# Performance work log

Measured on AMD Instinct MI355X. Metric: run time of the kernel, lower is better.

Reference implementation:

```python
import jax, jax.numpy as jnp
import numpy as np

EMBED = 1024
HEADS = 16
HEAD_DIM = EMBED // HEADS


def setup_inputs() -> dict:
    key = jax.random.key(0)
    ks = jax.random.split(key, 9)
    s = 0.02
    return {
        "hidden_states": jax.random.normal(ks[0], (1, 4, 1500, EMBED), dtype=jnp.float32),
        "q_w": jax.random.normal(ks[1], (EMBED, EMBED), dtype=jnp.float32) * s,
        "q_b": jax.random.normal(ks[2], (EMBED,), dtype=jnp.float32) * s,
        "k_w": jax.random.normal(ks[3], (EMBED, EMBED), dtype=jnp.float32) * s,
        "v_w": jax.random.normal(ks[4], (EMBED, EMBED), dtype=jnp.float32) * s,
        "v_b": jax.random.normal(ks[5], (EMBED,), dtype=jnp.float32) * s,
        "out_w": jax.random.normal(ks[6], (EMBED, EMBED), dtype=jnp.float32) * s,
        "out_b": jax.random.normal(ks[7], (EMBED,), dtype=jnp.float32) * s,
    }


def reference(hidden_states, q_w, q_b, k_w, v_w, v_b, out_w, out_b):
    # hidden_states: [1, B, S, E]
    _, bsz, tgt_len, _ = hidden_states.shape
    x = hidden_states[0]  # [B, S, E]
    scaling = HEAD_DIM ** -0.5

    def split_heads(t):  # [B, S, E] -> [B, H, S, Dh]
        return t.reshape(bsz, tgt_len, HEADS, HEAD_DIM).transpose(0, 2, 1, 3)

    # Linear layers use torch convention: y = x @ W.T + b  (k_proj has no bias)
    q = split_heads((x @ q_w.T + q_b) * scaling)
    k = split_heads(x @ k_w.T)
    v = split_heads(x @ v_w.T + v_b)

    # attention scores [B, H, S, S]
    attn_weights = jnp.einsum("bhqd,bhkd->bhqk", q, k)
    attn_probs = jax.nn.softmax(attn_weights, axis=-1)
    attn_out = jnp.einsum("bhqk,bhkd->bhqd", attn_probs, v)  # [B, H, S, Dh]

    attn_out = attn_out.transpose(0, 2, 1, 3).reshape(1, bsz, tgt_len, EMBED)
    return attn_out @ out_w.T + out_b
```

## Files before the change

### kernel.cpp

```cpp
#include <hip/hip_runtime.h>
#include <cstddef>
#include <cstdint>

#define EMB 1024
#define SEQ 1500
#define NB 4
#define NH 16
#define DH 64
#define MTOT (NB*SEQ)
#define VTS 1536

typedef __bf16 bf16;
typedef __bf16 bf16x4 __attribute__((ext_vector_type(4)));
typedef __bf16 bf16x8 __attribute__((ext_vector_type(8)));
typedef short  s16x4  __attribute__((ext_vector_type(4)));
typedef float  f32x4  __attribute__((ext_vector_type(4)));

#define LOG2E 1.44269504088896340736f

__device__ __forceinline__ void async16(const void* g, const void* l) {
    __builtin_amdgcn_global_load_lds(
        (const __attribute__((address_space(1))) uint32_t*)g,
        (__attribute__((address_space(3))) uint32_t*)l, 16, 0, 0);
}

__device__ __forceinline__ uint32_t pack_bf16_trunc(float e0, float e1) {
    return __builtin_amdgcn_perm(__builtin_bit_cast(uint32_t, e1),
                                 __builtin_bit_cast(uint32_t, e0), 0x07060302u);
}

struct CvtArgs {
    const float* xs; bf16* xd;
    const float* w[4]; bf16* wd[4];
};

__global__ __launch_bounds__(256) void cvt_kernel(CvtArgs a) {
    const size_t NX = (size_t)MTOT * EMB;
    const size_t NW = (size_t)EMB * EMB;
    const size_t tot = NX + 4 * NW;
    for (size_t i = ((size_t)blockIdx.x * 256 + threadIdx.x) * 4; i < tot;
         i += (size_t)gridDim.x * 1024) {
        const float* s; bf16* d; size_t off;
        if (i < NX) { s = a.xs; d = a.xd; off = i; }
        else {
            size_t j = i - NX;
            int wi = (int)(j >> 20);
            off = j & (NW - 1);
            s = a.w[wi]; d = a.wd[wi];
        }
        float4 v = *(const float4*)(s + off);
        bf16x4 o = { (bf16)v.x, (bf16)v.y, (bf16)v.z, (bf16)v.w };
        *(bf16x4*)(d + off) = o;
    }
}

__global__ __launch_bounds__(256) void gemm_fused(
    const bf16* __restrict__ X,
    const bf16* __restrict__ W0, const bf16* __restrict__ W1, const bf16* __restrict__ W2,
    const float* __restrict__ b_q, const float* __restrict__ b_v,
    bf16* __restrict__ Oq, bf16* __restrict__ Ok, bf16* __restrict__ Ovt,
    int M)
{
    __shared__ bf16 As[2][128 * 32];
    __shared__ bf16 Bs[2][128 * 32];
    const int tid = threadIdx.x;
    const int lane = tid & 63, w = tid >> 6;
    const int q = lane >> 4, lr = lane & 15;
    const int wr = w >> 1, wc = w & 1;

    const int id = blockIdx.x;
    const int t_ = id >> 3;
    const int mtile = (id & 7) + (t_ % 6) * 8;
    const int y = t_ / 6;
    const int m0 = mtile * 128;
    const int proj = y >> 3;
    const int n0 = (y & 7) * 128;

    const bf16 *PA, *PB;
    int baseA, baseB, limA, limB;
    if (proj == 2) {
        PA = X;  baseA = m0; limA = M;
        PB = W2; baseB = n0; limB = EMB;
    } else {
        PA = (proj == 0) ? W0 : W1;
        baseA = n0; limA = EMB;
        PB = X; baseB = m0; limB = M;
    }

    f32x4 acc[4][4] = {};

    const int srow = w * 32 + (lane >> 2);
    const int swz_ch = (((lane & 3) ^ ((lane >> 3) & 3))) * 8;
    const bf16* pA[2]; const bf16* pB[2];
#pragma unroll
    for (int i = 0; i < 2; i++) {
        int ra = baseA + srow + i * 16; ra = ra < limA ? ra : limA - 1;
        int rb = baseB + srow + i * 16; rb = rb < limB ? rb : limB - 1;
        pA[i] = PA + (size_t)ra * EMB + swz_ch;
        pB[i] = PB + (size_t)rb * EMB + swz_ch;
    }

#pragma unroll
    for (int i = 0; i < 2; i++) {
        async16(pA[i], As[0] + (w * 2 + i) * 512);
        async16(pB[i], Bs[0] + (w * 2 + i) * 512);
    }

    const int qsw = (q ^ ((lr >> 1) & 3)) * 8;
    const int arow = (wr * 64 + lr) * 32;
    const int brow = (wc * 64 + lr) * 32;

    for (int k0 = 0; k0 < EMB; k0 += 32) {
        const int cur = (k0 >> 5) & 1;
        __syncthreads();
        const int nxt = k0 + 32;
        if (nxt < EMB) {
#pragma unroll
            for (int i = 0; i < 2; i++) {
                async16(pA[i] + nxt, As[cur ^ 1] + (w * 2 + i) * 512);
                async16(pB[i] + nxt, Bs[cur ^ 1] + (w * 2 + i) * 512);
            }
        }
        const bf16* Ab = As[cur];
        const bf16* Bb = Bs[cur];
        bf16x8 af[4], bfr[4];
#pragma unroll
        for (int t = 0; t < 4; t++) {
            af[t]  = *(const bf16x8*)(Ab + arow + t * 512 + qsw);
            bfr[t] = *(const bf16x8*)(Bb + brow + t * 512 + qsw);
        }
#pragma unroll
        for (int ti = 0; ti < 4; ti++)
#pragma unroll
            for (int tj = 0; tj < 4; tj++)
                acc[ti][tj] = __builtin_amdgcn_mfma_f32_16x16x32_bf16(
                    af[ti], bfr[tj], acc[ti][tj], 0, 0, 0);
    }

    if (proj <= 1) {
        const float scale = (proj == 0) ? 0.125f * LOG2E : 1.0f;
        const float* bias = (proj == 0) ? b_q : nullptr;
        bf16* O = (proj == 0) ? Oq : Ok;
#pragma unroll
        for (int tj = 0; tj < 4; tj++) {
            const int m = m0 + wc * 64 + tj * 16 + lr;
            if (m >= M) continue;
            const int b_ = m / SEQ, s_ = m % SEQ;
#pragma unroll
            for (int ti = 0; ti < 4; ti++) {
                const int nb = n0 + wr * 64 + ti * 16 + q * 4;
                const int h = nb >> 6, d = nb & 63;
                float4 b4 = bias ? *(const float4*)(bias + nb)
                                 : make_float4(0.f, 0.f, 0.f, 0.f);
                bf16x4 o;
                o[0] = (bf16)((acc[ti][tj][0] + b4.x) * scale);
                o[1] = (bf16)((acc[ti][tj][1] + b4.y) * scale);
                o[2] = (bf16)((acc[ti][tj][2] + b4.z) * scale);
                o[3] = (bf16)((acc[ti][tj][3] + b4.w) * scale);
                *(bf16x4*)(O + (((size_t)b_ * NH + h) * SEQ + s_) * DH + d) = o;
            }
        }
    } else {
#pragma unroll
        for (int ti = 0; ti < 4; ti++) {
            const int mb = m0 + wr * 64 + ti * 16 + q * 4;
            if (mb >= M) continue;
            const int b_ = mb / SEQ, s_ = mb % SEQ;
#pragma unroll
            for (int tj = 0; tj < 4; tj++) {
                const int nb = n0 + wc * 64 + tj * 16 + lr;
                const int h = nb >> 6, d = nb & 63;
                const float bv = b_v[nb];
                bf16x4 o;
                o[0] = (bf16)(acc[ti][tj][0] + bv);
                o[1] = (bf16)(acc[ti][tj][1] + bv);
                o[2] = (bf16)(acc[ti][tj][2] + bv);
                o[3] = (bf16)(acc[ti][tj][3] + bv);
                *(bf16x4*)(Ovt + ((size_t)(b_ * NH + h) * DH + d) * VTS + s_) = o;
            }
        }
    }
}

__global__ __launch_bounds__(256) void gemm_out(
    const bf16* __restrict__ X, const bf16* __restrict__ Wo,
    const float* __restrict__ b_o, float* __restrict__ Of, int M)
{
    __shared__ bf16 As[2][64 * 32];
    __shared__ bf16 Bs[2][128 * 32];
    const int tid = threadIdx.x;
    const int lane = tid & 63, w = tid >> 6;
    const int q = lane >> 4, lr = lane & 15;
    const int wc = w & 1, wr = w >> 1;

    const int id = blockIdx.x;
    const int xcd = id & 7;
    const int h = id >> 3;
    const int mtile = (h % 6) * 8 + xcd;
    const int ntile = h / 6;
    const int m0 = mtile * 128, n0 = ntile * 64;

    const int cs = ((tid & 3) ^ ((tid >> 3) & 3)) * 8;
    const bf16* pA = Wo + (size_t)(n0 + (tid >> 2)) * EMB + cs;
    const int srow = w * 32 + (lane >> 2);
    const bf16* pB[2];
#pragma unroll
    for (int i = 0; i < 2; i++) {
        int rb = m0 + srow + i * 16; rb = rb < M ? rb : M - 1;
        pB[i] = X + (size_t)rb * EMB + cs;
    }

    async16(pA, As[0] + w * 512);
#pragma unroll
    for (int i = 0; i < 2; i++)
        async16(pB[i], Bs[0] + (w * 2 + i) * 512);

    f32x4 acc[2][4] = {};
    const int qsw = (q ^ ((lr >> 1) & 3)) * 8;
    const int arow = (wr * 32 + lr) * 32;
    const int brow = (wc * 64 + lr) * 32;

    for (int k0 = 0; k0 < EMB; k0 += 32) {
        const int cur = (k0 >> 5) & 1;
        __syncthreads();
        const int nxt = k0 + 32;
        if (nxt < EMB) {
            async16(pA + nxt, As[cur ^ 1] + w * 512);
#pragma unroll
            for (int i = 0; i < 2; i++)
                async16(pB[i] + nxt, Bs[cur ^ 1] + (w * 2 + i) * 512);
        }
        bf16x8 af[2], bfr[4];
#pragma unroll
        for (int t = 0; t < 2; t++)
            af[t] = *(const bf16x8*)(As[cur] + arow + t * 512 + qsw);
#pragma unroll
        for (int t = 0; t < 4; t++)
            bfr[t] = *(const bf16x8*)(Bs[cur] + brow + t * 512 + qsw);
#pragma unroll
        for (int ti = 0; ti < 2; ti++)
#pragma unroll
            for (int tj = 0; tj < 4; tj++)
                acc[ti][tj] = __builtin_amdgcn_mfma_f32_16x16x32_bf16(
                    af[ti], bfr[tj], acc[ti][tj], 0, 0, 0);
    }

#pragma unroll
    for (int tj = 0; tj < 4; tj++) {
        const int m = m0 + wc * 64 + tj * 16 + lr;
        if (m >= M) continue;
#pragma unroll
        for (int ti = 0; ti < 2; ti++) {
            const int nb = n0 + wr * 32 + ti * 16 + q * 4;
            const float4 b4 = *(const float4*)(b_o + nb);
            float4 o;
            o.x = acc[ti][tj][0] + b4.x;
            o.y = acc[ti][tj][1] + b4.y;
            o.z = acc[ti][tj][2] + b4.z;
            o.w = acc[ti][tj][3] + b4.w;
            *(float4*)(Of + (size_t)m * EMB + nb) = o;
        }
    }
}

#define QG 3
__global__ __launch_bounds__(256) void attn_mfma(
    const bf16* __restrict__ Qb, const bf16* __restrict__ Kb,
    const bf16* __restrict__ Vt, bf16* __restrict__ ctx)
{
    __shared__ bf16 Ks[2][64 * 64];
    __shared__ bf16 Vs[2][64 * 64];
    const int tid = threadIdx.x;
    const int lane = tid & 63, w = tid >> 6;
    const int q = lane >> 4, lr = lane & 15;
    const int bh = blockIdx.x, b_ = bh >> 4, h_ = bh & 15;
    const int q0 = blockIdx.y * (QG * 64);
    const size_t base = (size_t)bh * SEQ * DH;
    const size_t vbase = (size_t)bh * DH * VTS;

    int qrow[QG];
    bf16x8 qf[QG][2];
#pragma unroll
    for (int g = 0; g < QG; g++) {
        qrow[g] = q0 + g * 64 + w * 16 + lr;
        const int qrc = qrow[g] < SEQ ? qrow[g] : (SEQ - 1);
        qf[g][0] = *(const bf16x8*)(Qb + base + (size_t)qrc * DH + q * 8);
        qf[g][1] = *(const bf16x8*)(Qb + base + (size_t)qrc * DH + 32 + q * 8);
    }

    f32x4 oacc[QG][4] = {};
    f32x4 lacc[QG] = {};
    const s16x4 ones = { (short)0x3F80, (short)0x3F80, (short)0x3F80, (short)0x3F80 };

    const int srow = tid >> 3;
    const int sch8 = ((tid & 7) ^ (srow & 7)) * 8;
    const int kswz = lr & 7;

    const int NT = (SEQ + 63) / 64;

    {
        int r0 = srow, r1 = srow + 32;
        async16(Kb + base + (size_t)r0 * DH + sch8, Ks[0] + tid * 8);
        async16(Kb + base + (size_t)r1 * DH + sch8, Ks[0] + tid * 8 + 2048);
        async16(Vt + vbase + (size_t)srow * VTS + sch8,        Vs[0] + tid * 8);
        async16(Vt + vbase + (size_t)(srow + 32) * VTS + sch8, Vs[0] + tid * 8 + 2048);
    }

    for (int kt = 0; kt < NT; kt++) {
        const int k0 = kt * 64;
        const int cur = kt & 1;
        __syncthreads();

        if (kt + 1 < NT) {
            const int kn = k0 + 64;
            int r0 = kn + srow;      if (r0 >= SEQ) r0 = SEQ - 1;
            int r1 = kn + srow + 32; if (r1 >= SEQ) r1 = SEQ - 1;
            async16(Kb + base + (size_t)r0 * DH + sch8, Ks[cur ^ 1] + tid * 8);
            async16(Kb + base + (size_t)r1 * DH + sch8, Ks[cur ^ 1] + tid * 8 + 2048);
            async16(Vt + vbase + (size_t)srow * VTS + kn + sch8,
                    Vs[cur ^ 1] + tid * 8);
            async16(Vt + vbase + (size_t)(srow + 32) * VTS + kn + sch8,
                    Vs[cur ^ 1] + tid * 8 + 2048);
        }

        const bf16* Kc = Ks[cur];
        const bf16* Vc = Vs[cur];

        bf16x8 kf[2][4];
#pragma unroll
        for (int s = 0; s < 2; s++)
#pragma unroll
            for (int mt = 0; mt < 4; mt++)
                kf[s][mt] = *(const bf16x8*)(Kc + (mt * 16 + lr) * 64 +
                                             ((4 * s + q) ^ kswz) * 8);

        s16x4 pf[QG][4];
#pragma unroll
        for (int g = 0; g < QG; g++) {
            f32x4 st[4] = {};
#pragma unroll
            for (int s = 0; s < 2; s++)
#pragma unroll
                for (int mt = 0; mt < 4; mt++)
                    st[mt] = __builtin_amdgcn_mfma_f32_16x16x32_bf16(
                        kf[s][mt], qf[g][s], st[mt], 0, 0, 0);

            if (k0 + 64 > SEQ) {
#pragma unroll
                for (int mt = 0; mt < 4; mt++)
#pragma unroll
                    for (int r = 0; r < 4; r++)
                        if (k0 + mt * 16 + q * 4 + r >= SEQ) st[mt][r] = -16384.0f;
            }

#pragma unroll
            for (int mt = 0; mt < 4; mt++) {
                float e0 = __builtin_amdgcn_exp2f(st[mt][0]);
                float e1 = __builtin_amdgcn_exp2f(st[mt][1]);
                float e2 = __builtin_amdgcn_exp2f(st[mt][2]);
                float e3 = __builtin_amdgcn_exp2f(st[mt][3]);
                uint32_t lo = pack_bf16_trunc(e0, e1);
                uint32_t hi = pack_bf16_trunc(e2, e3);
                uint2 pk = { lo, hi };
                pf[g][mt] = __builtin_bit_cast(s16x4, pk);
            }
#pragma unroll
            for (int c = 0; c < 4; c++)
                lacc[g] = __builtin_amdgcn_mfma_f32_16x16x16bf16_1k(
                    ones, pf[g][c], lacc[g], 0, 0, 0);
        }

#pragma unroll
        for (int c = 0; c < 4; c++) {
#pragma unroll
            for (int dt = 0; dt < 4; dt++) {
                const s16x4 vf = __builtin_bit_cast(s16x4,
                    *(const bf16x4*)(Vc + (dt * 16 + lr) * 64 +
                                     ((2 * c + (q >> 1)) ^ kswz) * 8 + (q & 1) * 4));
#pragma unroll
                for (int g = 0; g < QG; g++)
                    oacc[g][dt] = __builtin_amdgcn_mfma_f32_16x16x16bf16_1k(
                        vf, pf[g][c], oacc[g][dt], 0, 0, 0);
            }
        }
    }

#pragma unroll
    for (int g = 0; g < QG; g++) {
        const float inv = 1.0f / lacc[g][0];
        if (qrow[g] < SEQ) {
            const size_t rowoff = ((size_t)b_ * SEQ + qrow[g]) * EMB + h_ * DH;
#pragma unroll
            for (int dt = 0; dt < 4; dt++) {
                bf16x4 o;
#pragma unroll
                for (int r = 0; r < 4; r++) o[r] = (bf16)(oacc[g][dt][r] * inv);
                *(bf16x4*)(ctx + rowoff + dt * 16 + q * 4) = o;
            }
        }
    }
}

extern "C" void kernel_launch(void* const* d_in, const int* in_sizes, int n_in,
                              void* d_out, int out_size, void* d_ws, size_t ws_size,
                              hipStream_t stream) {
    const float* x     = (const float*)d_in[0];
    const float* q_w   = (const float*)d_in[1];
    const float* q_b   = (const float*)d_in[2];
    const float* k_w   = (const float*)d_in[3];
    const float* v_w   = (const float*)d_in[4];
    const float* v_b   = (const float*)d_in[5];
    const float* out_w = (const float*)d_in[6];
    const float* out_b = (const float*)d_in[7];
    float* out = (float*)d_out;

    const size_t nbuf = (size_t)MTOT * EMB;
    const size_t nvt  = (size_t)NB * NH * DH * VTS;
    const size_t nw   = (size_t)EMB * EMB;
    bf16* xb  = (bf16*)d_ws;
    bf16* qws = xb  + nbuf;
    bf16* kws = qws + nbuf;
    bf16* vtw = kws + nbuf;
    bf16* wqb = vtw + nvt;
    bf16* wkb = wqb + nw;
    bf16* wvb = wkb + nw;
    bf16* wob = wvb + nw;
    bf16* ctx = xb;

    CvtArgs ca;
    ca.xs = x;      ca.xd = xb;
    ca.w[0] = q_w;  ca.wd[0] = wqb;
    ca.w[1] = k_w;  ca.wd[1] = wkb;
    ca.w[2] = v_w;  ca.wd[2] = wvb;
    ca.w[3] = out_w; ca.wd[3] = wob;
    cvt_kernel<<<dim3(2560), 256, 0, stream>>>(ca);

    gemm_fused<<<dim3(48 * 24), 256, 0, stream>>>(
        xb, wqb, wkb, wvb, q_b, v_b, qws, kws, vtw, MTOT);

    attn_mfma<<<dim3(NB * NH, (SEQ + QG * 64 - 1) / (QG * 64)), 256, 0, stream>>>(
        qws, kws, vtw, ctx);

    gemm_out<<<dim3(768), 256, 0, stream>>>(ctx, wob, out_b, out, MTOT);
}
```

Baseline: 240.0 us.

## Rewrite QKV projection GEMM with 256x256 tiles and 8-wave ping-pong pipeline

The fused QKV projection GEMM moves from 128x128 tiles with 4 waves and K-step 32 to 256x256 tiles with 8 waves and K-step 64. Loads use an XOR-swizzled LDS layout with double buffering per half-tile, and explicit barriers and vmcnt waits interleave global-to-LDS staging with MFMA bursts under raised priority. The larger tile is meant to raise data reuse and MFMA density and to hide load latency. In exchange it uses far more LDS and registers (128 accumulator floats per thread) and launches only 288 blocks, so the grid covers the CUs unevenly and the tail of the M dimension wastes work.

```diff
diff --git a/kernel.cpp b/kernel.cpp
--- a/kernel.cpp
+++ b/kernel.cpp
@@ -54,27 +54,28 @@
     }
 }
 
-__global__ __launch_bounds__(256) void gemm_fused(
+__global__ __launch_bounds__(512, 2) void gemm_fused(
     const bf16* __restrict__ X,
     const bf16* __restrict__ W0, const bf16* __restrict__ W1, const bf16* __restrict__ W2,
     const float* __restrict__ b_q, const float* __restrict__ b_v,
     bf16* __restrict__ Oq, bf16* __restrict__ Ok, bf16* __restrict__ Ovt,
     int M)
 {
-    __shared__ bf16 As[2][128 * 32];
-    __shared__ bf16 Bs[2][128 * 32];
+    __shared__ bf16 As[2][2][8192];
+    __shared__ bf16 Bs[2][2][8192];
+
     const int tid = threadIdx.x;
     const int lane = tid & 63, w = tid >> 6;
     const int q = lane >> 4, lr = lane & 15;
-    const int wr = w >> 1, wc = w & 1;
+    const int wa = w >> 2;
+    const int wb = w & 3;
 
     const int id = blockIdx.x;
-    const int t_ = id >> 3;
-    const int mtile = (id & 7) + (t_ % 6) * 8;
-    const int y = t_ / 6;
-    const int m0 = mtile * 128;
-    const int proj = y >> 3;
-    const int n0 = (y & 7) * 128;
+    const int mtile = (id & 7) + ((id >> 3) % 3) * 8;
+    const int y = (id >> 3) / 3;
+    const int proj = y >> 2;
+    const int n0 = (y & 3) * 256;
+    const int m0 = mtile * 256;
 
     const bf16 *PA, *PB;
     int baseA, baseB, limA, limB;
@@ -87,95 +88,159 @@
         PB = X; baseB = m0; limB = M;
     }
 
-    f32x4 acc[4][4] = {};
-
-    const int srow = w * 32 + (lane >> 2);
-    const int swz_ch = (((lane & 3) ^ ((lane >> 3) & 3))) * 8;
-    const bf16* pA[2]; const bf16* pB[2];
-#pragma unroll
-    for (int i = 0; i < 2; i++) {
-        int ra = baseA + srow + i * 16; ra = ra < limA ? ra : limA - 1;
-        int rb = baseB + srow + i * 16; rb = rb < limB ? rb : limB - 1;
-        pA[i] = PA + (size_t)ra * EMB + swz_ch;
-        pB[i] = PB + (size_t)rb * EMB + swz_ch;
-    }
-
-#pragma unroll
-    for (int i = 0; i < 2; i++) {
-        async16(pA[i], As[0] + (w * 2 + i) * 512);
-        async16(pB[i], Bs[0] + (w * 2 + i) * 512);
-    }
-
-    const int qsw = (q ^ ((lr >> 1) & 3)) * 8;
-    const int arow = (wr * 64 + lr) * 32;
-    const int brow = (wc * 64 + lr) * 32;
-
-    for (int k0 = 0; k0 < EMB; k0 += 32) {
-        const int cur = (k0 >> 5) & 1;
-        __syncthreads();
-        const int nxt = k0 + 32;
-        if (nxt < EMB) {
-#pragma unroll
-            for (int i = 0; i < 2; i++) {
-                async16(pA[i] + nxt, As[cur ^ 1] + (w * 2 + i) * 512);
-                async16(pB[i] + nxt, Bs[cur ^ 1] + (w * 2 + i) * 512);
-            }
-        }
-        const bf16* Ab = As[cur];
-        const bf16* Bb = Bs[cur];
-        bf16x8 af[4], bfr[4];
-#pragma unroll
-        for (int t = 0; t < 4; t++) {
-            af[t]  = *(const bf16x8*)(Ab + arow + t * 512 + qsw);
-            bfr[t] = *(const bf16x8*)(Bb + brow + t * 512 + qsw);
-        }
-#pragma unroll
-        for (int ti = 0; ti < 4; ti++)
-#pragma unroll
-            for (int tj = 0; tj < 4; tj++)
-                acc[ti][tj] = __builtin_amdgcn_mfma_f32_16x16x32_bf16(
-                    af[ti], bfr[tj], acc[ti][tj], 0, 0, 0);
-    }
+    const int srow = tid >> 3;
+    const int sch  = ((tid & 7) ^ ((tid >> 3) & 7)) * 8;
+    const bf16* gA[2][2]; const bf16* gB[2][2];
+#pragma unroll
+    for (int h = 0; h < 2; h++)
+#pragma unroll
+        for (int i = 0; i < 2; i++) {
+            int ra = baseA + h * 128 + i * 64 + srow; ra = ra < limA ? ra : limA - 1;
+            int rb = baseB + h * 128 + i * 64 + srow; rb = rb < limB ? rb : limB - 1;
+            gA[h][i] = PA + (size_t)ra * EMB + sch;
+            gB[h][i] = PB + (size_t)rb * EMB + sch;
+        }
+
+#define STAGE_AH(buf, h, kt) do { \
+    async16(gA[h][0] + (kt) * 64, &As[buf][h][w * 512]); \
+    async16(gA[h][1] + (kt) * 64, &As[buf][h][4096 + w * 512]); } while (0)
+#define STAGE_BH(buf, h, kt) do { \
+    async16(gB[h][0] + (kt) * 64, &Bs[buf][h][w * 512]); \
+    async16(gB[h][1] + (kt) * 64, &Bs[buf][h][4096 + w * 512]); } while (0)
+
+#define BAR() asm volatile("s_barrier" ::: "memory")
+#define VMC4() asm volatile("s_waitcnt vmcnt(4)" ::: "memory")
+#define VMC0() asm volatile("s_waitcnt vmcnt(0)" ::: "memory")
+
+    const int xoff0 = (((q * 16)      ^ ((lr & 7) << 4)) >> 1);
+    const int xoff1 = (((64 + q * 16) ^ ((lr & 7) << 4)) >> 1);
+
+    const bf16* Ab0 = &As[0][wa][0];
+    const bf16* Ab1 = &As[1][wa][0];
+    const bf16* Bb0 = &Bs[0][wb >> 1][(wb & 1) * 4096];
+    const bf16* Bb1 = &Bs[1][wb >> 1][(wb & 1) * 4096];
+
+    f32x4  acc[8][4] = {};
+    bf16x8 a[4][2], b0[2][2], b1[2][2];
+
+#define READ_A(P, qa) do { _Pragma("unroll") \
+    for (int f = 0; f < 4; f++) { \
+        a[f][0] = *(const bf16x8*)((P) + ((qa) * 4 + f) * 1024 + lr * 64 + xoff0); \
+        a[f][1] = *(const bf16x8*)((P) + ((qa) * 4 + f) * 1024 + lr * 64 + xoff1); } } while (0)
+#define READ_B(P, qb, br) do { _Pragma("unroll") \
+    for (int g = 0; g < 2; g++) { \
+        br[g][0] = *(const bf16x8*)((P) + ((qb) * 2 + g) * 1024 + lr * 64 + xoff0); \
+        br[g][1] = *(const bf16x8*)((P) + ((qb) * 2 + g) * 1024 + lr * 64 + xoff1); } } while (0)
+#define MFMA16(qa, qb, br) do { \
+    __builtin_amdgcn_s_setprio(1); \
+    _Pragma("unroll") for (int f = 0; f < 4; f++) \
+    _Pragma("unroll") for (int g = 0; g < 2; g++) { \
+        acc[(qa)*4+f][(qb)*2+g] = __builtin_amdgcn_mfma_f32_16x16x32_bf16( \
+            a[f][0], br[g][0], acc[(qa)*4+f][(qb)*2+g], 0, 0, 0); \
+        acc[(qa)*4+f][(qb)*2+g] = __builtin_amdgcn_mfma_f32_16x16x32_bf16( \
+            a[f][1], br[g][1], acc[(qa)*4+f][(qb)*2+g], 0, 0, 0); } \
+    __builtin_amdgcn_s_setprio(0); } while (0)
+
+    STAGE_BH(0, 0, 0); STAGE_BH(0, 1, 0);
+    STAGE_AH(0, 0, 0); STAGE_AH(0, 1, 0);
+    STAGE_BH(1, 0, 1); STAGE_BH(1, 1, 1);
+    VMC4();
+    BAR();
+
+    for (int it = 0; it < 8; ++it) {
+        const int T1 = 2 * it + 1, T2 = 2 * it + 2, T3 = 2 * it + 3;
+        const bool more = (it < 7);
+
+        READ_A(Ab0, 0); READ_B(Bb0, 0, b0);
+        STAGE_AH(1, 0, T1);
+        BAR();
+        MFMA16(0, 0, b0);
+        BAR();
+        READ_B(Bb0, 1, b1);
+        STAGE_AH(1, 1, T1);
+        BAR();
+        MFMA16(0, 1, b1);
+        BAR();
+        READ_A(Ab0, 1);
+        if (more) STAGE_BH(0, 0, T2);
+        BAR();
+        MFMA16(1, 1, b1);
+        BAR();
+        if (more) STAGE_AH(0, 0, T2);
+        BAR();
+        MFMA16(1, 0, b0);
+        if (more) { VMC4(); } else { VMC0(); }
+        BAR();
+        READ_A(Ab1, 0); READ_B(Bb1, 0, b0);
+        if (more) STAGE_BH(0, 1, T2);
+        BAR();
+        MFMA16(0, 0, b0);
+        BAR();
+        READ_B(Bb1, 1, b1);
+        if (more) STAGE_AH(0, 1, T2);
+        BAR();
+        MFMA16(0, 1, b1);
+        BAR();
+        READ_A(Ab1, 1);
+        if (more) STAGE_BH(1, 0, T3);
+        BAR();
+        MFMA16(1, 1, b1);
+        BAR();
+        if (more) STAGE_BH(1, 1, T3);
+        BAR();
+        MFMA16(1, 0, b0);
+        if (more) VMC4();
+        BAR();
+    }
+
+#undef STAGE_AH
+#undef STAGE_BH
+#undef BAR
+#undef VMC4
+#undef VMC0
+#undef READ_A
+#undef READ_B
+#undef MFMA16
 
     if (proj <= 1) {
         const float scale = (proj == 0) ? 0.125f * LOG2E : 1.0f;
         const float* bias = (proj == 0) ? b_q : nullptr;
         bf16* O = (proj == 0) ? Oq : Ok;
 #pragma unroll
-        for (int tj = 0; tj < 4; tj++) {
-            const int m = m0 + wc * 64 + tj * 16 + lr;
+        for (int bn = 0; bn < 4; bn++) {
+            const int m = m0 + wb * 64 + bn * 16 + lr;
             if (m >= M) continue;
             const int b_ = m / SEQ, s_ = m % SEQ;
 #pragma unroll
-            for (int ti = 0; ti < 4; ti++) {
-                const int nb = n0 + wr * 64 + ti * 16 + q * 4;
+            for (int am = 0; am < 8; am++) {
+                const int nb = n0 + wa * 128 + am * 16 + q * 4;
                 const int h = nb >> 6, d = nb & 63;
                 float4 b4 = bias ? *(const float4*)(bias + nb)
                                  : make_float4(0.f, 0.f, 0.f, 0.f);
                 bf16x4 o;
-                o[0] = (bf16)((acc[ti][tj][0] + b4.x) * scale);
-                o[1] = (bf16)((acc[ti][tj][1] + b4.y) * scale);
-                o[2] = (bf16)((acc[ti][tj][2] + b4.z) * scale);
-                o[3] = (bf16)((acc[ti][tj][3] + b4.w) * scale);
+                o[0] = (bf16)((acc[am][bn][0] + b4.x) * scale);
+                o[1] = (bf16)((acc[am][bn][1] + b4.y) * scale);
+                o[2] = (bf16)((acc[am][bn][2] + b4.z) * scale);
+                o[3] = (bf16)((acc[am][bn][3] + b4.w) * scale);
                 *(bf16x4*)(O + (((size_t)b_ * NH + h) * SEQ + s_) * DH + d) = o;
             }
         }
     } else {
 #pragma unroll
-        for (int ti = 0; ti < 4; ti++) {
-            const int mb = m0 + wr * 64 + ti * 16 + q * 4;
+        for (int am = 0; am < 8; am++) {
+            const int mb = m0 + wa * 128 + am * 16 + q * 4;
             if (mb >= M) continue;
             const int b_ = mb / SEQ, s_ = mb % SEQ;
 #pragma unroll
-            for (int tj = 0; tj < 4; tj++) {
-                const int nb = n0 + wc * 64 + tj * 16 + lr;
+            for (int bn = 0; bn < 4; bn++) {
+                const int nb = n0 + wb * 64 + bn * 16 + lr;
                 const int h = nb >> 6, d = nb & 63;
                 const float bv = b_v[nb];
                 bf16x4 o;
-                o[0] = (bf16)(acc[ti][tj][0] + bv);
-                o[1] = (bf16)(acc[ti][tj][1] + bv);
-                o[2] = (bf16)(acc[ti][tj][2] + bv);
-                o[3] = (bf16)(acc[ti][tj][3] + bv);
+                o[0] = (bf16)(acc[am][bn][0] + bv);
+                o[1] = (bf16)(acc[am][bn][1] + bv);
+                o[2] = (bf16)(acc[am][bn][2] + bv);
+                o[3] = (bf16)(acc[am][bn][3] + bv);
                 *(bf16x4*)(Ovt + ((size_t)(b_ * NH + h) * DH + d) * VTS + s_) = o;
             }
         }
@@ -435,7 +500,7 @@
     ca.w[3] = out_w; ca.wd[3] = wob;
     cvt_kernel<<<dim3(2560), 256, 0, stream>>>(ca);
 
-    gemm_fused<<<dim3(48 * 24), 256, 0, stream>>>(
+    gemm_fused<<<dim3(288), 512, 0, stream>>>(
         xb, wqb, wkb, wvb, q_b, v_b, qws, kws, vtw, MTOT);
 
     attn_mfma<<<dim3(NB * NH, (SEQ + QG * 64 - 1) / (QG * 64)), 256, 0, stream>>>(
```

Result: slower. 250.9 us (+4.5%).
